# Performance work log

Hardware: AMD Instinct MI355X
Metric: run time of the kernel (lower is better)

Reference implementation:

```python
import jax, jax.numpy as jnp
import numpy as np

DATA_DIM = 10000
ID_EMBED_DIM = 256
QK_DIM = 64
B, N = 4, 4096
SCALE = QK_DIM ** (-0.5)


def setup_inputs() -> dict:
    key = jax.random.key(0)
    k1, k2, k3, k4, k5, k6, k7 = jax.random.split(key, 7)
    val = jax.random.normal(k1, (B, N), dtype=jnp.float32)
    pos = jax.random.randint(k2, (B, N), 0, DATA_DIM + 1)
    # learned params (torch default inits approximated with scaled normals/uniforms)
    embed = jax.random.normal(k3, (DATA_DIM + 1, ID_EMBED_DIM), dtype=jnp.float32)
    lim = 1.0 / np.sqrt(ID_EMBED_DIM)
    Wq = jax.random.uniform(k4, (QK_DIM, ID_EMBED_DIM), minval=-lim, maxval=lim, dtype=jnp.float32)
    bq = jax.random.uniform(k5, (QK_DIM,), minval=-lim, maxval=lim, dtype=jnp.float32)
    Wk = jax.random.uniform(k6, (QK_DIM, ID_EMBED_DIM), minval=-lim, maxval=lim, dtype=jnp.float32)
    bk = jax.random.uniform(k7, (QK_DIM,), minval=-lim, maxval=lim, dtype=jnp.float32)
    return {"t": 0, "val": val, "pos": pos, "embed": embed,
            "Wq": Wq, "bq": bq, "Wk": Wk, "bk": bk}


def reference(t, val, pos, embed, Wq, bq, Wk, bk):
    # t is unused (ODE-style signature)
    id_embed = embed[pos]                              # [B, N, E] gather
    q = jnp.einsum('bne,de->bnd', id_embed, Wq) + bq   # [B, N, D]
    k = jnp.einsum('bne,de->bnd', id_embed, Wk) + bk   # [B, N, D]
    # soft_weights[b,i,j] = q[b,i,:] . k[b,j,:] * scale  (no softmax)
    soft_weights = jnp.einsum('bid,bjd->bij', q, k) * SCALE  # [B, N, N]
    fx = jnp.einsum('bij,bi->bj', soft_weights, val)         # contract over i
    return val + val * fx
```

## Files before the change

kernel.cpp:

```cpp
#include <hip/hip_runtime.h>

#define NN 4096
#define BB 4
#define EE 256
#define DD 64
#define SCALE 0.125f
#define NBLK 128
#define RB 32
#define RW 8

__global__ __launch_bounds__(256) void k_accum(
        const float* __restrict__ val, const int* __restrict__ pos,
        const float* __restrict__ embed,
        float* __restrict__ part, float* __restrict__ vpart) {
    const int b = blockIdx.y, t = threadIdx.x;
    const int lane = t & 63, wv = t >> 6;
    const int base = b * NN + blockIdx.x * RB + wv * RW;

    float v[RW]; int p[RW];
    #pragma unroll
    for (int r = 0; r < RW; ++r) { v[r] = val[base + r]; p[r] = pos[base + r]; }

    float4 acc = make_float4(0.f, 0.f, 0.f, 0.f);
    float vs = 0.f;
    #pragma unroll
    for (int r = 0; r < RW; ++r) {
        const float4 ev = reinterpret_cast<const float4*>(embed + (size_t)p[r] * EE)[lane];
        acc.x += v[r] * ev.x; acc.y += v[r] * ev.y;
        acc.z += v[r] * ev.z; acc.w += v[r] * ev.w;
        vs += v[r];
    }

    __shared__ float plds[4][EE];
    __shared__ float vlds[4];
    *reinterpret_cast<float4*>(&plds[wv][4 * lane]) = acc;
    if (lane == 0) vlds[wv] = vs;
    __syncthreads();

    const float s = plds[0][t] + plds[1][t] + plds[2][t] + plds[3][t];
    part[((size_t)b * NBLK + blockIdx.x) * EE + t] = s;
    if (t == 0) vpart[b * NBLK + blockIdx.x] = vlds[0] + vlds[1] + vlds[2] + vlds[3];
}

__global__ __launch_bounds__(256) void k_fused(
        const float* __restrict__ val, const int* __restrict__ pos,
        const float* __restrict__ embed,
        const float* __restrict__ part, const float* __restrict__ vpart,
        const float* __restrict__ Wq, const float* __restrict__ bq,
        const float* __restrict__ Wk, const float* __restrict__ bk,
        float* __restrict__ out) {
    const int b = blockIdx.y, t = threadIdx.x;
    const int lane = t & 63, wv = t >> 6;

    __shared__ float uS[EE];
    __shared__ float ps[4][DD];
    __shared__ float sS[DD];
    __shared__ float wsh[EE];
    __shared__ float rowres[RB];
    __shared__ float cSh, vS;

    {
        float a = 0.f;
        const float* pp = part + (size_t)b * NBLK * EE + t;
        #pragma unroll 8
        for (int blk = 0; blk < NBLK; ++blk) a += pp[(size_t)blk * EE];
        uS[t] = a;
    }
    if (t < 64) {
        float x = vpart[b * NBLK + lane] + vpart[b * NBLK + 64 + lane];
        #pragma unroll
        for (int off = 32; off; off >>= 1) x += __shfl_down(x, off, 64);
        if (lane == 0) vS = x;
    }
    __syncthreads();

    {
        const int d = lane, seg = wv;
        const float4* uu = reinterpret_cast<const float4*>(&uS[seg * 64]);
        const float4* wq = reinterpret_cast<const float4*>(Wq + (size_t)d * EE + seg * 64);
        float a = 0.f;
        #pragma unroll
        for (int q = 0; q < 16; ++q) {
            const float4 x = uu[q], y = wq[q];
            a += x.x * y.x + x.y * y.y + x.z * y.z + x.w * y.w;
        }
        ps[seg][d] = a;
    }
    __syncthreads();
    if (t < DD) sS[t] = ps[0][t] + ps[1][t] + ps[2][t] + ps[3][t] + bq[t] * vS;
    __syncthreads();

    if (wv == 0) {
        float x = sS[lane] * bk[lane];
        #pragma unroll
        for (int off = 32; off; off >>= 1) x += __shfl_down(x, off, 64);
        if (lane == 0) cSh = x;
    }
    {
        float a = 0.f;
        #pragma unroll
        for (int d = 0; d < DD; ++d) a += sS[d] * Wk[d * EE + t];
        wsh[t] = a;
    }
    __syncthreads();

    const float4 wf = reinterpret_cast<const float4*>(wsh)[lane];
    const int base = b * NN + blockIdx.x * RB + wv * RW;
    int p[RW];
    #pragma unroll
    for (int r = 0; r < RW; ++r) p[r] = pos[base + r];
    #pragma unroll
    for (int r = 0; r < RW; ++r) {
        const float4 ev = reinterpret_cast<const float4*>(embed + (size_t)p[r] * EE)[lane];
        float a = ev.x * wf.x + ev.y * wf.y + ev.z * wf.z + ev.w * wf.w;
        #pragma unroll
        for (int off = 32; off; off >>= 1) a += __shfl_down(a, off, 64);
        if (lane == 0) rowres[wv * RW + r] = a;
    }
    __syncthreads();
    if (t < RB) {
        const int j = blockIdx.x * RB + t;
        const float v = val[b * NN + j];
        out[b * NN + j] = v * (1.f + SCALE * (rowres[t] + cSh));
    }
}

extern "C" void kernel_launch(void* const* d_in, const int* in_sizes, int n_in,
                              void* d_out, int out_size, void* d_ws, size_t ws_size,
                              hipStream_t stream) {
    const float* val   = (const float*)d_in[1];
    const int*   pos   = (const int*)d_in[2];
    const float* embed = (const float*)d_in[3];
    const float* Wq    = (const float*)d_in[4];
    const float* bq    = (const float*)d_in[5];
    const float* Wk    = (const float*)d_in[6];
    const float* bk    = (const float*)d_in[7];
    float* out = (float*)d_out;

    float* part  = (float*)d_ws;
    float* vpart = part + (size_t)BB * NBLK * EE;

    dim3 g(NBLK, BB);
    k_accum<<<g, 256, 0, stream>>>(val, pos, embed, part, vpart);
    k_fused<<<g, 256, 0, stream>>>(val, pos, embed, part, vpart, Wq, bq, Wk, bk, out);
}
```

Baseline: 91.56 us.

## Fuse accumulate and output kernels into one cooperative kernel with grid sync

Merges the two kernels into one cooperative launch that uses a grid-wide barrier. Each block now projects its own partial embedding sum through Wq before the barrier, so only 64-wide partials go through global memory instead of 256-wide ones. The gathered embedding rows stay in registers across the barrier, so the second gather pass is gone. The cost is the grid-sync overhead and a cooperative launch that requires all 512 blocks to be resident at once.

```diff
diff --git a/kernel.cpp b/kernel.cpp
--- a/kernel.cpp
+++ b/kernel.cpp
@@ -1,4 +1,7 @@
 #include <hip/hip_runtime.h>
+#include <hip/hip_cooperative_groups.h>
+
+namespace cg = cooperative_groups;
 
 #define NN 4096
 #define BB 4
@@ -9,73 +12,54 @@
 #define RB 32
 #define RW 8
 
-__global__ __launch_bounds__(256) void k_accum(
+__global__ __launch_bounds__(256) void k_all(
         const float* __restrict__ val, const int* __restrict__ pos,
         const float* __restrict__ embed,
-        float* __restrict__ part, float* __restrict__ vpart) {
-    const int b = blockIdx.y, t = threadIdx.x;
-    const int lane = t & 63, wv = t >> 6;
-    const int base = b * NN + blockIdx.x * RB + wv * RW;
+        const float* __restrict__ Wq, const float* __restrict__ bq,
+        const float* __restrict__ Wk, const float* __restrict__ bk,
+        float* __restrict__ part_s, float* __restrict__ out) {
+    const int b    = blockIdx.y;
+    const int bx   = blockIdx.x;
+    const int t    = threadIdx.x;
+    const int lane = t & 63;
+    const int wv   = t >> 6;
+    const int seg  = wv;
+    const int base = b * NN + bx * RB + wv * RW;
+
+    __shared__ float plds[4][EE];
+    __shared__ float vlds[4];
+    __shared__ float uS[EE];
+    __shared__ float ps[4][DD];
+    __shared__ float sS[DD];
+    __shared__ float wsh[EE];
+    __shared__ float rowres[RB];
+    __shared__ float cSh;
 
     float v[RW]; int p[RW];
     #pragma unroll
     for (int r = 0; r < RW; ++r) { v[r] = val[base + r]; p[r] = pos[base + r]; }
 
+    float4 ev[RW];
+    #pragma unroll
+    for (int r = 0; r < RW; ++r)
+        ev[r] = reinterpret_cast<const float4*>(embed + (size_t)p[r] * EE)[lane];
+
     float4 acc = make_float4(0.f, 0.f, 0.f, 0.f);
     float vs = 0.f;
     #pragma unroll
     for (int r = 0; r < RW; ++r) {
-        const float4 ev = reinterpret_cast<const float4*>(embed + (size_t)p[r] * EE)[lane];
-        acc.x += v[r] * ev.x; acc.y += v[r] * ev.y;
-        acc.z += v[r] * ev.z; acc.w += v[r] * ev.w;
+        acc.x += v[r] * ev[r].x; acc.y += v[r] * ev[r].y;
+        acc.z += v[r] * ev[r].z; acc.w += v[r] * ev[r].w;
         vs += v[r];
     }
-
-    __shared__ float plds[4][EE];
-    __shared__ float vlds[4];
     *reinterpret_cast<float4*>(&plds[wv][4 * lane]) = acc;
     if (lane == 0) vlds[wv] = vs;
     __syncthreads();
-
-    const float s = plds[0][t] + plds[1][t] + plds[2][t] + plds[3][t];
-    part[((size_t)b * NBLK + blockIdx.x) * EE + t] = s;
-    if (t == 0) vpart[b * NBLK + blockIdx.x] = vlds[0] + vlds[1] + vlds[2] + vlds[3];
-}
-
-__global__ __launch_bounds__(256) void k_fused(
-        const float* __restrict__ val, const int* __restrict__ pos,
-        const float* __restrict__ embed,
-        const float* __restrict__ part, const float* __restrict__ vpart,
-        const float* __restrict__ Wq, const float* __restrict__ bq,
-        const float* __restrict__ Wk, const float* __restrict__ bk,
-        float* __restrict__ out) {
-    const int b = blockIdx.y, t = threadIdx.x;
-    const int lane = t & 63, wv = t >> 6;
-
-    __shared__ float uS[EE];
-    __shared__ float ps[4][DD];
-    __shared__ float sS[DD];
-    __shared__ float wsh[EE];
-    __shared__ float rowres[RB];
-    __shared__ float cSh, vS;
-
-    {
-        float a = 0.f;
-        const float* pp = part + (size_t)b * NBLK * EE + t;
-        #pragma unroll 8
-        for (int blk = 0; blk < NBLK; ++blk) a += pp[(size_t)blk * EE];
-        uS[t] = a;
-    }
-    if (t < 64) {
-        float x = vpart[b * NBLK + lane] + vpart[b * NBLK + 64 + lane];
-        #pragma unroll
-        for (int off = 32; off; off >>= 1) x += __shfl_down(x, off, 64);
-        if (lane == 0) vS = x;
-    }
+    uS[t] = plds[0][t] + plds[1][t] + plds[2][t] + plds[3][t];
     __syncthreads();
 
     {
-        const int d = lane, seg = wv;
+        const int d = lane;
         const float4* uu = reinterpret_cast<const float4*>(&uS[seg * 64]);
         const float4* wq = reinterpret_cast<const float4*>(Wq + (size_t)d * EE + seg * 64);
         float a = 0.f;
@@ -87,7 +71,24 @@
         ps[seg][d] = a;
     }
     __syncthreads();
-    if (t < DD) sS[t] = ps[0][t] + ps[1][t] + ps[2][t] + ps[3][t] + bq[t] * vS;
+    if (t < DD) {
+        const float Vblk = vlds[0] + vlds[1] + vlds[2] + vlds[3];
+        part_s[((size_t)b * NBLK + bx) * DD + t] =
+            ps[0][t] + ps[1][t] + ps[2][t] + ps[3][t] + bq[t] * Vblk;
+    }
+
+    cg::this_grid().sync();
+
+    {
+        const int d = lane;
+        const float* pp = part_s + ((size_t)b * NBLK + seg * 32) * DD + d;
+        float a = 0.f;
+        #pragma unroll 8
+        for (int i = 0; i < 32; ++i) a += pp[(size_t)i * DD];
+        ps[seg][d] = a;
+    }
+    __syncthreads();
+    if (t < DD) sS[t] = ps[0][t] + ps[1][t] + ps[2][t] + ps[3][t];
     __syncthreads();
 
     if (wv == 0) {
@@ -105,23 +106,18 @@
     __syncthreads();
 
     const float4 wf = reinterpret_cast<const float4*>(wsh)[lane];
-    const int base = b * NN + blockIdx.x * RB + wv * RW;
-    int p[RW];
-    #pragma unroll
-    for (int r = 0; r < RW; ++r) p[r] = pos[base + r];
     #pragma unroll
     for (int r = 0; r < RW; ++r) {
-        const float4 ev = reinterpret_cast<const float4*>(embed + (size_t)p[r] * EE)[lane];
-        float a = ev.x * wf.x + ev.y * wf.y + ev.z * wf.z + ev.w * wf.w;
+        float a = ev[r].x * wf.x + ev[r].y * wf.y + ev[r].z * wf.z + ev[r].w * wf.w;
         #pragma unroll
         for (int off = 32; off; off >>= 1) a += __shfl_down(a, off, 64);
         if (lane == 0) rowres[wv * RW + r] = a;
     }
     __syncthreads();
     if (t < RB) {
-        const int j = blockIdx.x * RB + t;
-        const float v = val[b * NN + j];
-        out[b * NN + j] = v * (1.f + SCALE * (rowres[t] + cSh));
+        const int j = bx * RB + t;
+        const float vv = val[b * NN + j];
+        out[b * NN + j] = vv * (1.f + SCALE * (rowres[t] + cSh));
     }
 }
 
@@ -135,12 +131,12 @@
     const float* bq    = (const float*)d_in[5];
     const float* Wk    = (const float*)d_in[6];
     const float* bk    = (const float*)d_in[7];
-    float* out = (float*)d_out;
+    float* out    = (float*)d_out;
+    float* part_s = (float*)d_ws;
 
-    float* part  = (float*)d_ws;
-    float* vpart = part + (size_t)BB * NBLK * EE;
-
-    dim3 g(NBLK, BB);
-    k_accum<<<g, 256, 0, stream>>>(val, pos, embed, part, vpart);
-    k_fused<<<g, 256, 0, stream>>>(val, pos, embed, part, vpart, Wq, bq, Wk, bk, out);
+    void* args[] = { (void*)&val, (void*)&pos, (void*)&embed,
+                     (void*)&Wq, (void*)&bq, (void*)&Wk, (void*)&bk,
+                     (void*)&part_s, (void*)&out };
+    dim3 grid(NBLK, BB);
+    hipLaunchCooperativeKernel((const void*)k_all, grid, dim3(256), args, 0, stream);
 }
```

Measured after the change: 136.0 us. 48.5% more time.
